# Performance work log

Measured on AMD Instinct MI355X. Metric: run time of the kernel, lower is better.

## Reference

```python
import jax, jax.numpy as jnp
import numpy as np

HEADS = 8
N_NODES = 16384
DIM = 256
NUM_GLOBAL = 4
E_LOCAL = 131072
E_EXP = 65536


def setup_inputs() -> dict:
    key = jax.random.key(0)
    ks = jax.random.split(key, 8)
    x = jax.random.normal(ks[0], (N_NODES, DIM), dtype=jnp.float32)
    edge_index = jax.random.randint(ks[1], (2, E_LOCAL), 0, N_NODES)
    expander_edge_index = jax.random.randint(ks[2], (2, E_EXP), 0, N_NODES)
    W_qkv = jax.random.normal(ks[3], (DIM, 3 * DIM), dtype=jnp.float32) * (DIM ** -0.5)
    b_qkv = jax.random.normal(ks[4], (3 * DIM,), dtype=jnp.float32) * 0.01
    W_out = jax.random.normal(ks[5], (DIM, DIM), dtype=jnp.float32) * (DIM ** -0.5)
    b_out = jax.random.normal(ks[6], (DIM,), dtype=jnp.float32) * 0.01
    global_tokens = jax.random.normal(ks[7], (NUM_GLOBAL, DIM), dtype=jnp.float32)
    return {"x": x, "edge_index": edge_index,
            "expander_edge_index": expander_edge_index,
            "W_qkv": W_qkv, "b_qkv": b_qkv,
            "W_out": W_out, "b_out": b_out,
            "global_tokens": global_tokens}


def _build_edges(edge_index, expander_edge_index, N, G):
    # local edges + self loops (PyG add_self_loops appends [i,i] edges)
    self_loops = jnp.arange(N)
    nodes = jnp.arange(N)
    gids = jnp.arange(N, N + G)
    # node -> global: meshgrid(arange(N), global_nodes, 'ij') -> src node repeated, dst global tiled
    n2g_src = jnp.repeat(nodes, G)
    n2g_dst = jnp.tile(gids, N)
    src = jnp.concatenate([edge_index[0], self_loops, expander_edge_index[0], n2g_src, n2g_dst])
    dst = jnp.concatenate([edge_index[1], self_loops, expander_edge_index[1], n2g_dst, n2g_src])
    return src, dst


def reference(x, edge_index, expander_edge_index, W_qkv, b_qkv, W_out, b_out, global_tokens):
    N, dim = x.shape
    G = global_tokens.shape[0]
    H = HEADS
    D = dim // H
    total = N + G

    x_full = jnp.concatenate([x, global_tokens], axis=0)          # [N+G, dim]
    qkv = (x_full @ W_qkv + b_qkv).reshape(total, 3, H, D)
    Q, K, V = qkv[:, 0], qkv[:, 1], qkv[:, 2]                     # [N+G, H, D]

    src, dst = _build_edges(edge_index, expander_edge_index, N, G)  # [E]

    scale = D ** -0.5
    scores = (Q[dst] * K[src]).sum(axis=-1) * scale               # [E, H]

    # segment softmax over destination nodes
    m = jax.ops.segment_max(scores, dst, num_segments=total)      # [N+G, H]
    e = jnp.exp(scores - m[dst])                                  # [E, H]
    denom = jax.ops.segment_sum(e, dst, num_segments=total)       # [N+G, H]
    attn = e / denom[dst]                                         # [E, H]

    # scatter-weighted V sum (index_add over dst)
    out = jax.ops.segment_sum(attn[:, :, None] * V[src], dst, num_segments=total)  # [N+G, H, D]
    out = out[:N].reshape(N, H * D)
    return out @ W_out + b_out
```

## Files before the change

kernel.cpp:

```cpp
#include <hip/hip_runtime.h>
#include <hip/hip_bf16.h>
#include <stdint.h>

#define N_NODES   16384
#define DIMM      256
#define HEADS     8
#define HDIM      32
#define NUM_GLOBAL 4
#define N_TOT     (N_NODES + NUM_GLOBAL)
#define E_LOCAL   131072
#define E_EXP     65536
#define E_CSR     (E_LOCAL + E_EXP)
#define ADJ_CAP   64

typedef __hip_bfloat16 bf16;
typedef __attribute__((ext_vector_type(8))) short short8;
typedef __attribute__((ext_vector_type(4))) short sh4;
typedef __attribute__((ext_vector_type(4))) float f32x4;

__device__ __forceinline__ short f2s(float f) {
    bf16 h = __float2bfloat16(f);
    return __builtin_bit_cast(short, h);
}
__device__ __forceinline__ float bu2f(unsigned short u) {
    return __bfloat162float(__builtin_bit_cast(bf16, u));
}

__device__ __forceinline__ int swz(int c, int r) {
    return c ^ (r & 7) ^ ((r >> 3) & 7);
}

__global__ __launch_bounds__(256) void prep_kernel(
    const float* __restrict__ Wqkv, const float* __restrict__ Wout,
    const int* __restrict__ ei, const int* __restrict__ xei,
    const float* __restrict__ x, const float* __restrict__ gtok,
    bf16* __restrict__ Wt1, bf16* __restrict__ Wt2,
    int* __restrict__ cnt, unsigned short* __restrict__ adjP, bf16* __restrict__ Xb)
{
    const int b = blockIdx.x;
    const int t = threadIdx.x;
    if (b < 64) {
        __shared__ float T[64][65];
        const float* src; bf16* dst; int n0, k0, ldn;
        if (b < 48) { src = Wqkv; dst = Wt1; n0 = (b % 12) * 64; k0 = (b / 12) * 64; ldn = 768; }
        else        { int bb = b - 48; src = Wout; dst = Wt2; n0 = (bb & 3) * 64; k0 = (bb >> 2) * 64; ldn = 256; }
        #pragma unroll
        for (int i = 0; i < 4; ++i) {
            int idx = t + 256 * i;
            int r = idx >> 4, c4 = (idx & 15) * 4;
            float4 v = *(const float4*)(src + (size_t)(k0 + r) * ldn + n0 + c4);
            T[r][c4] = v.x; T[r][c4 + 1] = v.y; T[r][c4 + 2] = v.z; T[r][c4 + 3] = v.w;
        }
        __syncthreads();
        #pragma unroll
        for (int i = 0; i < 4; ++i) {
            int idx = t + 256 * i;
            int nr = idx >> 4, kk = (idx & 15) * 4;
            sh4 o;
            o[0] = f2s(T[kk][nr]);     o[1] = f2s(T[kk + 1][nr]);
            o[2] = f2s(T[kk + 2][nr]); o[3] = f2s(T[kk + 3][nr]);
            *(sh4*)(dst + (size_t)(n0 + nr) * 256 + k0 + kk) = o;
        }
    } else if (b < 832) {
        int e = (b - 64) * 256 + t;
        int s, d;
        if (e < E_LOCAL)      { s = ei[e];            d = ei[E_LOCAL + e]; }
        else if (e < E_CSR)   { int ee = e - E_LOCAL; s = xei[ee]; d = xei[E_EXP + ee]; }
        else return;
        int pos = atomicAdd(&cnt[d], 1);
        if (pos < ADJ_CAP) adjP[(d << 6) + pos] = (unsigned short)s;
    } else {
        int e0 = ((b - 832) * 256 + t) * 8;
        if (e0 < N_TOT * DIMM) {
            int row = e0 >> 8, col = e0 & 255;
            const float* p = (row < N_NODES)
                ? x + (size_t)row * DIMM + col
                : gtok + (size_t)(row - N_NODES) * DIMM + col;
            float4 v0 = *(const float4*)p, v1 = *(const float4*)(p + 4);
            short8 o;
            o[0] = f2s(v0.x); o[1] = f2s(v0.y); o[2] = f2s(v0.z); o[3] = f2s(v0.w);
            o[4] = f2s(v1.x); o[5] = f2s(v1.y); o[6] = f2s(v1.z); o[7] = f2s(v1.w);
            *(short8*)((short*)Xb + (size_t)row * DIMM + col) = o;
        }
    }
}

__global__ __launch_bounds__(256) void qkv_mfma(
    const bf16* __restrict__ Xb, const bf16* __restrict__ Wt,
    const float* __restrict__ bias,
    bf16* __restrict__ Qb, bf16* __restrict__ KVh)
{
    const int b = blockIdx.x;
    const int xcd = b & 7;
    const int i = b >> 3;
    const int mt = xcd + 8 * (i / 6);
    if (mt >= 129) return;
    const int m0 = mt * 128;
    const int n0 = (i % 6) * 128;

    __shared__ __align__(16) short SM[32768];
    const int t  = threadIdx.x;
    const int wid = t >> 6, lane = t & 63;
    const int wr = wid >> 1, wc = wid & 1;
    const int lm = lane & 15, lq = lane >> 4;

    f32x4 acc[4][4] = {};
    short8 aregs[4];

    int sr[4], skc[4];
    #pragma unroll
    for (int ii = 0; ii < 4; ++ii) {
        int c8 = t + 256 * ii;
        sr[ii] = c8 >> 3; skc[ii] = c8 & 7;
    }

    #pragma unroll
    for (int ii = 0; ii < 4; ++ii)
        aregs[ii] = *(const short8*)((const short*)Xb + (size_t)(m0 + sr[ii]) * DIMM + skc[ii] * 8);
    #pragma unroll
    for (int ii = 0; ii < 4; ++ii)
        *(short8*)(SM + sr[ii] * 64 + swz(skc[ii], sr[ii]) * 8) = aregs[ii];
    #pragma unroll
    for (int ii = 0; ii < 4; ++ii) {
        short8 v = *(const short8*)((const short*)Wt + (size_t)(n0 + sr[ii]) * 256 + skc[ii] * 8);
        *(short8*)(SM + 8192 + sr[ii] * 64 + swz(skc[ii], sr[ii]) * 8) = v;
    }
    __syncthreads();

    #pragma unroll
    for (int tstep = 0; tstep < 4; ++tstep) {
        const int p = tstep & 1;
        short* As = SM + p * 16384;
        short* Bs = As + 8192;
        if (tstep < 3) {
            const int kn = (tstep + 1) * 64;
            #pragma unroll
            for (int ii = 0; ii < 4; ++ii)
                aregs[ii] = *(const short8*)((const short*)Xb + (size_t)(m0 + sr[ii]) * DIMM + kn + skc[ii] * 8);
        }
        #pragma unroll
        for (int kk = 0; kk < 2; ++kk) {
            const int c = kk * 4 + lq;
            short8 af[4], bfq[4];
            #pragma unroll
            for (int mi = 0; mi < 4; ++mi) {
                int r = wr * 64 + mi * 16 + lm;
                af[mi] = *(const short8*)(As + r * 64 + swz(c, r) * 8);
            }
            #pragma unroll
            for (int ni = 0; ni < 4; ++ni) {
                int n = wc * 64 + ni * 16 + lm;
                bfq[ni] = *(const short8*)(Bs + n * 64 + swz(c, n) * 8);
            }
            #pragma unroll
            for (int mi = 0; mi < 4; ++mi)
                #pragma unroll
                for (int ni = 0; ni < 4; ++ni)
                    acc[mi][ni] = __builtin_amdgcn_mfma_f32_16x16x32_bf16(
                        af[mi], bfq[ni], acc[mi][ni], 0, 0, 0);
        }
        if (tstep < 3) {
            const int kn = (tstep + 1) * 64;
            short* An = SM + (1 - p) * 16384;
            short* Bn = An + 8192;
            __syncthreads();
            #pragma unroll
            for (int ii = 0; ii < 4; ++ii)
                *(short8*)(An + sr[ii] * 64 + swz(skc[ii], sr[ii]) * 8) = aregs[ii];
            #pragma unroll
            for (int ii = 0; ii < 4; ++ii) {
                short8 v = *(const short8*)((const short*)Wt + (size_t)(n0 + sr[ii]) * 256 + kn + skc[ii] * 8);
                *(short8*)(Bn + sr[ii] * 64 + swz(skc[ii], sr[ii]) * 8) = v;
            }
            __syncthreads();
        }
    }

    __syncthreads();
    #pragma unroll
    for (int ni = 0; ni < 4; ++ni) {
        int col = wc * 64 + ni * 16 + lm;
        float bv = bias[n0 + col];
        #pragma unroll
        for (int mi = 0; mi < 4; ++mi) {
            int rowb = wr * 64 + mi * 16 + lq * 4;
            #pragma unroll
            for (int rr = 0; rr < 4; ++rr)
                SM[(rowb + rr) * 136 + col] = f2s(acc[mi][ni][rr] + bv);
        }
    }
    __syncthreads();
    #pragma unroll
    for (int it = 0; it < 8; ++it) {
        int idx = it * 256 + t;
        int r = idx >> 4, c8 = idx & 15;
        int row = m0 + r;
        if (row < N_TOT) {
            int colbase = n0 + (c8 >> 3) * 64;
            int sel = colbase >> 8;
            int cc = (colbase & 255) + (c8 & 7) * 8;
            short8 v = *(const short8*)(SM + r * 136 + c8 * 8);
            short* dp;
            if (sel == 0) {
                dp = (short*)Qb + (size_t)row * DIMM + cc;
            } else {
                int head = cc >> 5, dim = cc & 31;
                dp = (short*)KVh + ((size_t)head * N_TOT + row) * 64 + (sel - 1) * 32 + dim;
            }
            *(short8*)dp = v;
        }
    }
}

__global__ __launch_bounds__(256) void out_mfma(
    const bf16* __restrict__ O, const bf16* __restrict__ Wt,
    const float* __restrict__ bias, float* __restrict__ out)
{
    const int b = blockIdx.x;
    const int xcd = b & 7;
    const int i = b >> 3;
    const int m0 = (xcd + 8 * (i >> 1)) * 128;
    const int n0 = (i & 1) * 128;

    __shared__ __align__(16) short SM[128 * 136];
    short* As = SM;
    short* Bs = SM + 128 * 64;
    float* CF = (float*)SM;
    const int t  = threadIdx.x;
    const int wid = t >> 6, lane = t & 63;
    const int wr = wid >> 1, wc = wid & 1;
    const int lm = lane & 15, lq = lane >> 4;

    f32x4 acc[4][4] = {};

    for (int k0 = 0; k0 < DIMM; k0 += 64) {
        if (k0) __syncthreads();
        #pragma unroll
        for (int ii = 0; ii < 4; ++ii) {
            int c8 = t + 256 * ii;
            int r  = c8 >> 3, kc = c8 & 7;
            short8 v = *(const short8*)((const short*)O + (size_t)(m0 + r) * DIMM + k0 + kc * 8);
            *(short8*)(As + r * 64 + swz(kc, r) * 8) = v;
        }
        #pragma unroll
        for (int ii = 0; ii < 4; ++ii) {
            int c8 = t + 256 * ii;
            int n  = c8 >> 3, kc = c8 & 7;
            short8 v = *(const short8*)((const short*)Wt + (size_t)(n0 + n) * 256 + k0 + kc * 8);
            *(short8*)(Bs + n * 64 + swz(kc, n) * 8) = v;
        }
        __syncthreads();
        #pragma unroll
        for (int kk = 0; kk < 2; ++kk) {
            const int c = kk * 4 + lq;
            short8 af[4], bfq[4];
            #pragma unroll
            for (int mi = 0; mi < 4; ++mi) {
                int r = wr * 64 + mi * 16 + lm;
                af[mi] = *(const short8*)(As + r * 64 + swz(c, r) * 8);
            }
            #pragma unroll
            for (int ni = 0; ni < 4; ++ni) {
                int n = wc * 64 + ni * 16 + lm;
                bfq[ni] = *(const short8*)(Bs + n * 64 + swz(c, n) * 8);
            }
            #pragma unroll
            for (int mi = 0; mi < 4; ++mi)
                #pragma unroll
                for (int ni = 0; ni < 4; ++ni)
                    acc[mi][ni] = __builtin_amdgcn_mfma_f32_16x16x32_bf16(
                        af[mi], bfq[ni], acc[mi][ni], 0, 0, 0);
        }
    }

    #pragma unroll
    for (int p = 0; p < 2; ++p) {
        __syncthreads();
        if (wr == p) {
            #pragma unroll
            for (int ni = 0; ni < 4; ++ni) {
                int col = wc * 64 + ni * 16 + lm;
                float bv = bias[n0 + col];
                #pragma unroll
                for (int mi = 0; mi < 4; ++mi) {
                    int lr = mi * 16 + lq * 4;
                    #pragma unroll
                    for (int rr = 0; rr < 4; ++rr) {
                        float val = acc[mi][ni][rr] + bv;
                        val = fminf(fmaxf(val, -1e4f), 1e4f);
                        CF[(lr + rr) * 132 + col] = val;
                    }
                }
            }
        }
        __syncthreads();
        #pragma unroll
        for (int it = 0; it < 8; ++it) {
            int idx = it * 256 + t;
            int r = idx >> 5, c4 = idx & 31;
            float4 v = *(const float4*)(CF + r * 132 + c4 * 4);
            *(float4*)(out + (size_t)(m0 + p * 64 + r) * DIMM + n0 + c4 * 4) = v;
        }
    }
}

__global__ __launch_bounds__(256) void attn_kernel(
    const bf16* __restrict__ Qb, const bf16* __restrict__ KVh,
    const int* __restrict__ cnt, const unsigned short* __restrict__ adjP,
    bf16* __restrict__ Ob)
{
    const int b = blockIdx.x;
    const int head = b & 7;
    const int wid = threadIdx.x >> 6;
    const int lane = threadIdx.x & 63;
    const int n = (b >> 3) * 4 + wid;
    const int g = lane >> 3, j = lane & 7;
    const float scale = 0.1767766952966369f;

    const ushort4* KV4 = (const ushort4*)KVh + (size_t)head * N_TOT * 16;

    ushort4 qu = ((const ushort4*)Qb)[(size_t)n * 64 + head * 8 + j];
    float4 q;
    q.x = bu2f(qu.x) * scale; q.y = bu2f(qu.y) * scale;
    q.z = bu2f(qu.z) * scale; q.w = bu2f(qu.w) * scale;

    const int areg = adjP[(n << 6) + lane];
    const int deg = min(cnt[n], ADJ_CAP);
    const int tot = deg + 5;

    float4 acc = make_float4(0.f, 0.f, 0.f, 0.f);
    float dsum = 0.f;

    auto IDX = [&](int base, int& sv, float& ok) {
        int ii = base + g - 5;
        bool val = (ii < deg);
        int sg = __shfl(areg, ii & 63);
        int s  = (ii < 0) ? ((ii == -5) ? n : (N_NODES + ii + 4)) : sg;
        sv = val ? s : n;
        ok = val ? 1.f : 0.f;
    };

    int svA; float okA;
    IDX(0, svA, okA);
    ushort4 kA = KV4[(size_t)svA * 16 + j];
    ushort4 vA = KV4[(size_t)svA * 16 + 8 + j];

    int base = 0;
    while (true) {
        int svB; float okB; ushort4 kB, vB;
        const bool more = (base + 8 < tot);
        if (more) {
            IDX(base + 8, svB, okB);
            kB = KV4[(size_t)svB * 16 + j];
            vB = KV4[(size_t)svB * 16 + 8 + j];
        }
        {
            float p = q.x * bu2f(kA.x) + q.y * bu2f(kA.y)
                    + q.z * bu2f(kA.z) + q.w * bu2f(kA.w);
            p += __shfl_xor(p, 1);
            p += __shfl_xor(p, 2);
            p += __shfl_xor(p, 4);
            float wgt = okA * __expf(fminf(p, 80.f));
            dsum += wgt;
            acc.x += wgt * bu2f(vA.x);
            acc.y += wgt * bu2f(vA.y);
            acc.z += wgt * bu2f(vA.z);
            acc.w += wgt * bu2f(vA.w);
        }
        if (!more) break;
        base += 8;
        svA = svB; okA = okB; kA = kB; vA = vB;
    }

    #pragma unroll
    for (int m = 8; m <= 32; m <<= 1) {
        acc.x += __shfl_xor(acc.x, m);
        acc.y += __shfl_xor(acc.y, m);
        acc.z += __shfl_xor(acc.z, m);
        acc.w += __shfl_xor(acc.w, m);
        dsum  += __shfl_xor(dsum, m);
    }

    if (lane < 8) {
        float r = 1.0f / fmaxf(dsum, 1e-30f);
        ushort4 o;
        o.x = (unsigned short)__builtin_bit_cast(short, __float2bfloat16(fminf(fmaxf(acc.x * r, -500.f), 500.f)));
        o.y = (unsigned short)__builtin_bit_cast(short, __float2bfloat16(fminf(fmaxf(acc.y * r, -500.f), 500.f)));
        o.z = (unsigned short)__builtin_bit_cast(short, __float2bfloat16(fminf(fmaxf(acc.z * r, -500.f), 500.f)));
        o.w = (unsigned short)__builtin_bit_cast(short, __float2bfloat16(fminf(fmaxf(acc.w * r, -500.f), 500.f)));
        ((ushort4*)Ob)[(size_t)n * 64 + head * 8 + j] = o;
    }
}

extern "C" void kernel_launch(void* const* d_in, const int* in_sizes, int n_in,
                              void* d_out, int out_size, void* d_ws, size_t ws_size,
                              hipStream_t stream)
{
    const float* x    = (const float*)d_in[0];
    const int*   ei   = (const int*)d_in[1];
    const int*   xei  = (const int*)d_in[2];
    const float* Wqkv = (const float*)d_in[3];
    const float* bqkv = (const float*)d_in[4];
    const float* Wout = (const float*)d_in[5];
    const float* bout = (const float*)d_in[6];
    const float* gtok = (const float*)d_in[7];

    int* cnt  = (int*)d_ws;
    unsigned short* adjP = (unsigned short*)(cnt + N_NODES);
    uintptr_t fb = ((uintptr_t)(adjP + (size_t)N_NODES * ADJ_CAP) + 15) & ~(uintptr_t)15;
    bf16*  Qb  = (bf16*)fb;
    bf16*  KVh = Qb + (size_t)N_TOT * DIMM;
    bf16*  Ob  = KVh + (size_t)N_TOT * 512;
    bf16*  Wt1 = Ob + (size_t)N_NODES * DIMM;
    bf16*  Wt2 = Wt1 + 768 * 256;
    bf16*  Xb  = Wt2 + 256 * 256;

    hipMemsetAsync(cnt, 0, N_NODES * sizeof(int), stream);

    prep_kernel<<<2881, 256, 0, stream>>>(Wqkv, Wout, ei, xei, x, gtok, Wt1, Wt2, cnt, adjP, Xb);
    qkv_mfma<<<816, 256, 0, stream>>>(Xb, Wt1, bqkv, Qb, KVh);
    attn_kernel<<<(N_NODES / 4) * 8, 256, 0, stream>>>(Qb, KVh, cnt, adjP, Ob);
    out_mfma<<<256, 256, 0, stream>>>(Ob, Wt2, bout, (float*)d_out);
}
```

Measured before the change: 158.5 us.

## Pack K/V for head pairs and process two heads per wavefront in attention

The qkv GEMM epilogue now writes K and V in a layout that interleaves pairs of heads, giving 256-byte rows per node per head pair. The attention kernel handles two heads per block with 16-byte loads per lane, which halves the grid and the number of index shuffles and adjacency reads per head. In exchange each lane holds twice the registers and the per-lane dot product is longer, and the layout change has to be kept consistent between the producer and consumer kernels.

```diff
diff --git a/kernel.cpp b/kernel.cpp
--- a/kernel.cpp
+++ b/kernel.cpp
@@ -15,6 +15,7 @@
 
 typedef __hip_bfloat16 bf16;
 typedef __attribute__((ext_vector_type(8))) short short8;
+typedef __attribute__((ext_vector_type(8))) unsigned short ush8;
 typedef __attribute__((ext_vector_type(4))) short sh4;
 typedef __attribute__((ext_vector_type(4))) float f32x4;
 
@@ -88,7 +89,7 @@
 __global__ __launch_bounds__(256) void qkv_mfma(
     const bf16* __restrict__ Xb, const bf16* __restrict__ Wt,
     const float* __restrict__ bias,
-    bf16* __restrict__ Qb, bf16* __restrict__ KVh)
+    bf16* __restrict__ Qb, bf16* __restrict__ KVp)
 {
     const int b = blockIdx.x;
     const int xcd = b & 7;
@@ -205,7 +206,9 @@
                 dp = (short*)Qb + (size_t)row * DIMM + cc;
             } else {
                 int head = cc >> 5, dim = cc & 31;
-                dp = (short*)KVh + ((size_t)head * N_TOT + row) * 64 + (sel - 1) * 32 + dim;
+                int pr = head >> 1, sub = head & 1;
+                dp = (short*)KVp + ((size_t)pr * N_TOT + row) * 128
+                   + (sel - 1) * 64 + sub * 32 + dim;
             }
             *(short8*)dp = v;
         }
@@ -305,30 +308,31 @@
 }
 
 __global__ __launch_bounds__(256) void attn_kernel(
-    const bf16* __restrict__ Qb, const bf16* __restrict__ KVh,
+    const bf16* __restrict__ Qb, const bf16* __restrict__ KVp,
     const int* __restrict__ cnt, const unsigned short* __restrict__ adjP,
     bf16* __restrict__ Ob)
 {
     const int b = blockIdx.x;
-    const int head = b & 7;
+    const int pair = b & 3;
     const int wid = threadIdx.x >> 6;
     const int lane = threadIdx.x & 63;
-    const int n = (b >> 3) * 4 + wid;
+    const int n = (b >> 2) * 4 + wid;
     const int g = lane >> 3, j = lane & 7;
     const float scale = 0.1767766952966369f;
 
-    const ushort4* KV4 = (const ushort4*)KVh + (size_t)head * N_TOT * 16;
-
-    ushort4 qu = ((const ushort4*)Qb)[(size_t)n * 64 + head * 8 + j];
-    float4 q;
-    q.x = bu2f(qu.x) * scale; q.y = bu2f(qu.y) * scale;
-    q.z = bu2f(qu.z) * scale; q.w = bu2f(qu.w) * scale;
+    const unsigned short* KV = (const unsigned short*)KVp + (size_t)pair * N_TOT * 128;
+
+    const int hoff = (pair * 2 + (j >> 2)) * 32 + (j & 3) * 8;
+    ush8 qu = *(const ush8*)((const unsigned short*)Qb + (size_t)n * DIMM + hoff);
+    float qf[8];
+    #pragma unroll
+    for (int e = 0; e < 8; ++e) qf[e] = bu2f(qu[e]) * scale;
 
     const int areg = adjP[(n << 6) + lane];
     const int deg = min(cnt[n], ADJ_CAP);
     const int tot = deg + 5;
 
-    float4 acc = make_float4(0.f, 0.f, 0.f, 0.f);
+    float acc[8] = {0.f, 0.f, 0.f, 0.f, 0.f, 0.f, 0.f, 0.f};
     float dsum = 0.f;
 
     auto IDX = [&](int base, int& sv, float& ok) {
@@ -342,30 +346,29 @@
 
     int svA; float okA;
     IDX(0, svA, okA);
-    ushort4 kA = KV4[(size_t)svA * 16 + j];
-    ushort4 vA = KV4[(size_t)svA * 16 + 8 + j];
+    ush8 kA = *(const ush8*)(KV + (size_t)svA * 128 + j * 8);
+    ush8 vA = *(const ush8*)(KV + (size_t)svA * 128 + 64 + j * 8);
 
     int base = 0;
     while (true) {
-        int svB; float okB; ushort4 kB, vB;
+        int svB; float okB; ush8 kB, vB;
         const bool more = (base + 8 < tot);
         if (more) {
             IDX(base + 8, svB, okB);
-            kB = KV4[(size_t)svB * 16 + j];
-            vB = KV4[(size_t)svB * 16 + 8 + j];
+            kB = *(const ush8*)(KV + (size_t)svB * 128 + j * 8);
+            vB = *(const ush8*)(KV + (size_t)svB * 128 + 64 + j * 8);
         }
         {
-            float p = q.x * bu2f(kA.x) + q.y * bu2f(kA.y)
-                    + q.z * bu2f(kA.z) + q.w * bu2f(kA.w);
+            float p = qf[0] * bu2f(kA[0]) + qf[1] * bu2f(kA[1])
+                    + qf[2] * bu2f(kA[2]) + qf[3] * bu2f(kA[3])
+                    + qf[4] * bu2f(kA[4]) + qf[5] * bu2f(kA[5])
+                    + qf[6] * bu2f(kA[6]) + qf[7] * bu2f(kA[7]);
             p += __shfl_xor(p, 1);
             p += __shfl_xor(p, 2);
-            p += __shfl_xor(p, 4);
             float wgt = okA * __expf(fminf(p, 80.f));
             dsum += wgt;
-            acc.x += wgt * bu2f(vA.x);
-            acc.y += wgt * bu2f(vA.y);
-            acc.z += wgt * bu2f(vA.z);
-            acc.w += wgt * bu2f(vA.w);
+            #pragma unroll
+            for (int e = 0; e < 8; ++e) acc[e] += wgt * bu2f(vA[e]);
         }
         if (!more) break;
         base += 8;
@@ -374,21 +377,20 @@
 
     #pragma unroll
     for (int m = 8; m <= 32; m <<= 1) {
-        acc.x += __shfl_xor(acc.x, m);
-        acc.y += __shfl_xor(acc.y, m);
-        acc.z += __shfl_xor(acc.z, m);
-        acc.w += __shfl_xor(acc.w, m);
-        dsum  += __shfl_xor(dsum, m);
-    }
-
-    if (lane < 8) {
+        #pragma unroll
+        for (int e = 0; e < 8; ++e) acc[e] += __shfl_xor(acc[e], m);
+        dsum += __shfl_xor(dsum, m);
+    }
+
+    if (g == 0) {
         float r = 1.0f / fmaxf(dsum, 1e-30f);
-        ushort4 o;
-        o.x = (unsigned short)__builtin_bit_cast(short, __float2bfloat16(fminf(fmaxf(acc.x * r, -500.f), 500.f)));
-        o.y = (unsigned short)__builtin_bit_cast(short, __float2bfloat16(fminf(fmaxf(acc.y * r, -500.f), 500.f)));
-        o.z = (unsigned short)__builtin_bit_cast(short, __float2bfloat16(fminf(fmaxf(acc.z * r, -500.f), 500.f)));
-        o.w = (unsigned short)__builtin_bit_cast(short, __float2bfloat16(fminf(fmaxf(acc.w * r, -500.f), 500.f)));
-        ((ushort4*)Ob)[(size_t)n * 64 + head * 8 + j] = o;
+        ush8 o;
+        #pragma unroll
+        for (int e = 0; e < 8; ++e) {
+            float v = fminf(fmaxf(acc[e] * r, -500.f), 500.f);
+            o[e] = (unsigned short)__builtin_bit_cast(short, __float2bfloat16(v));
+        }
+        *(ush8*)((unsigned short*)Ob + (size_t)n * DIMM + hoff) = o;
     }
 }
 
@@ -409,8 +411,8 @@
     unsigned short* adjP = (unsigned short*)(cnt + N_NODES);
     uintptr_t fb = ((uintptr_t)(adjP + (size_t)N_NODES * ADJ_CAP) + 15) & ~(uintptr_t)15;
     bf16*  Qb  = (bf16*)fb;
-    bf16*  KVh = Qb + (size_t)N_TOT * DIMM;
-    bf16*  Ob  = KVh + (size_t)N_TOT * 512;
+    bf16*  KVp = Qb + (size_t)N_TOT * DIMM;
+    bf16*  Ob  = KVp + (size_t)N_TOT * 512;
     bf16*  Wt1 = Ob + (size_t)N_NODES * DIMM;
     bf16*  Wt2 = Wt1 + 768 * 256;
     bf16*  Xb  = Wt2 + 256 * 256;
@@ -418,7 +420,7 @@
     hipMemsetAsync(cnt, 0, N_NODES * sizeof(int), stream);
 
     prep_kernel<<<2881, 256, 0, stream>>>(Wqkv, Wout, ei, xei, x, gtok, Wt1, Wt2, cnt, adjP, Xb);
-    qkv_mfma<<<816, 256, 0, stream>>>(Xb, Wt1, bqkv, Qb, KVh);
-    attn_kernel<<<(N_NODES / 4) * 8, 256, 0, stream>>>(Qb, KVh, cnt, adjP, Ob);
+    qkv_mfma<<<816, 256, 0, stream>>>(Xb, Wt1, bqkv, Qb, KVp);
+    attn_kernel<<<(N_NODES / 4) * 4, 256, 0, stream>>>(Qb, KVp, cnt, adjP, Ob);
     out_mfma<<<256, 256, 0, stream>>>(Ob, Wt2, bout, (float*)d_out);
 }
```

New measurement: 146.1 us. -7.8%, faster.
